# Optimization experiments

Hardware: AMD Instinct MI355X
Metric: run time of the kernel (lower is better)

## Reference

```python
import jax, jax.numpy as jnp
import numpy as np

A0 = 0.5291772105638411
KE = 14.399645351950548


def _softplus_inverse(x):
    return x + np.log(-np.expm1(-x))


def _sigma(x):
    # exp(-1/clamp(x,1e-12)) underflows to 0 for x<=0, so the where is nan-free
    return jnp.where(x > 0, jnp.exp(-1.0 / jnp.maximum(x, 1e-12)), 0.0)


def _switch(x, x_on, x_off):
    c = (x - x_on) / (x_off - x_on)
    s1 = _sigma(1.0 - c)
    s0 = _sigma(c)
    return s1 / (s1 + s0 + 1e-12)


def setup_inputs() -> dict:
    key = jax.random.key(0)
    k0, k1, k2, k3, k4 = jax.random.split(key, 5)
    N = 100000
    E = 6400000
    atomic_numbers = jax.random.uniform(k0, (N,), jnp.float32, 1.0, 30.0)
    cutoffs = jax.random.uniform(k1, (E, 1), jnp.float32)
    lengths = jax.random.uniform(k2, (E, 1), jnp.float32, 0.5, 3.0)
    senders = jax.random.randint(k3, (E,), 0, N)
    receivers = jax.random.randint(k4, (E,), 0, N)
    init = dict(a1=3.2, a2=0.9423, a3=0.4028, a4=0.2016,
                c1=0.1818, c2=0.5099, c3=0.2802, c4=0.02817,
                p=0.23, d=1.0 / (0.8854 * A0))
    params = {k + '_raw': jnp.asarray([_softplus_inverse(v)], jnp.float32)
              for k, v in init.items()}
    out = {'atomic_numbers': atomic_numbers, 'cutoffs': cutoffs,
           'senders': senders, 'receivers': receivers,
           'lengths': lengths, 'num_nodes': N}
    out.update(params)
    return out


def reference(atomic_numbers, cutoffs, senders, receivers, lengths, num_nodes,
              a1_raw, a2_raw, a3_raw, a4_raw,
              c1_raw, c2_raw, c3_raw, c4_raw, p_raw, d_raw):
    sp = jax.nn.softplus
    a1, a2, a3, a4 = sp(a1_raw), sp(a2_raw), sp(a3_raw), sp(a4_raw)
    c1, c2, c3, c4 = sp(c1_raw), sp(c2_raw), sp(c3_raw), sp(c4_raw)
    p, d = sp(p_raw), sp(d_raw)
    c_sum = c1 + c2 + c3 + c4
    c1, c2, c3, c4 = c1 / c_sum, c2 / c_sum, c3 / c_sum, c4 / c_sum

    cut = cutoffs[:, 0]   # [E]
    L = lengths[:, 0]     # [E]
    z_i = atomic_numbers[receivers]
    z_j = atomic_numbers[senders]

    x = KE * cut * (z_i * z_j) / jnp.maximum(L, 1e-6)
    rzd = L * (jnp.power(z_i, p) + jnp.power(z_j, p)) * d
    y = (c1 * jnp.exp(-a1 * rzd) + c2 * jnp.exp(-a2 * rzd)
         + c3 * jnp.exp(-a3 * rzd) + c4 * jnp.exp(-a4 * rzd))
    w = _switch(L, 0.0, 1.5)
    e_rep_edge = w * x * y * 0.5
    return jax.ops.segment_sum(e_rep_edge, receivers, num_segments=num_nodes)[:, None]
```

## Files before the change

### kernel.cpp

```cpp
#include <hip/hip_runtime.h>
#include <math.h>

#define C0KE 7.199822675975274f
#define LOG2E 1.4426950408889634f
#define BSHIFT 8
#define NB 391
#define CAP 8192
#define PAIRS_OFF 2048
#define K1_BLOCKS 512
#define K1_THREADS 1024

__device__ __forceinline__ float softplusf(float x) {
    return (x > 20.0f) ? x : log1pf(__expf(x));
}

struct ZblParams { float A1, A2, A3, A4, c1, c2, c3, c4, p; };

__device__ __forceinline__ void load_params(
    const float* a1r, const float* a2r, const float* a3r, const float* a4r,
    const float* c1r, const float* c2r, const float* c3r, const float* c4r,
    const float* pr, const float* dr, ZblParams* P)
{
    float d  = softplusf(dr[0]);
    float s  = d * LOG2E;
    P->A1 = softplusf(a1r[0]) * s;
    P->A2 = softplusf(a2r[0]) * s;
    P->A3 = softplusf(a3r[0]) * s;
    P->A4 = softplusf(a4r[0]) * s;
    float c1 = softplusf(c1r[0]), c2 = softplusf(c2r[0]);
    float c3 = softplusf(c3r[0]), c4 = softplusf(c4r[0]);
    float inv = 1.0f / (c1 + c2 + c3 + c4);
    P->c1 = c1 * inv; P->c2 = c2 * inv; P->c3 = c3 * inv; P->c4 = c4 * inv;
    P->p = softplusf(pr[0]);
}

__device__ __forceinline__ float edge_energy_fast(
    float l, float cut_, float zi, float zj, const ZblParams& P)
{
    float c  = l * (1.0f / 1.5f);
    float om = 1.0f - c;
    float s1 = __builtin_amdgcn_exp2f(-LOG2E * __builtin_amdgcn_rcpf(om));
    float s0 = __builtin_amdgcn_exp2f(-LOG2E * __builtin_amdgcn_rcpf(c));
    float w  = s1 * __builtin_amdgcn_rcpf(s1 + s0);
    float x  = C0KE * cut_ * zi * zj * __builtin_amdgcn_rcpf(l);
    float S  = __builtin_amdgcn_exp2f(P.p * __builtin_amdgcn_logf(zi))
             + __builtin_amdgcn_exp2f(P.p * __builtin_amdgcn_logf(zj));
    float t  = l * S;
    float y  = P.c1 * __builtin_amdgcn_exp2f(-P.A1 * t)
             + P.c2 * __builtin_amdgcn_exp2f(-P.A2 * t)
             + P.c3 * __builtin_amdgcn_exp2f(-P.A3 * t)
             + P.c4 * __builtin_amdgcn_exp2f(-P.A4 * t);
    return w * x * y;
}

__global__ __launch_bounds__(K1_THREADS, 8) void zbl_scatter(
    const float* __restrict__ z, const float* __restrict__ cut,
    const int* __restrict__ snd, const int* __restrict__ rcv,
    const float* __restrict__ len,
    const float* __restrict__ a1r, const float* __restrict__ a2r,
    const float* __restrict__ a3r, const float* __restrict__ a4r,
    const float* __restrict__ c1r, const float* __restrict__ c2r,
    const float* __restrict__ c3r, const float* __restrict__ c4r,
    const float* __restrict__ pr,  const float* __restrict__ dr,
    float* __restrict__ out, unsigned* __restrict__ cursor,
    unsigned* __restrict__ pairs, int E)
{
    __shared__ ZblParams P;
    __shared__ unsigned hist[NB];
    __shared__ unsigned basearr[NB];

    for (int b = threadIdx.x; b < NB; b += blockDim.x) hist[b] = 0;
    if (threadIdx.x == 0)
        load_params(a1r, a2r, a3r, a4r, c1r, c2r, c3r, c4r, pr, dr, &P);
    __syncthreads();

    int nq = (E + 3) >> 2;
    int qpb = (nq + gridDim.x - 1) / gridDim.x;
    int q0 = blockIdx.x * qpb;
    int q1 = min(q0 + qpb, nq);

    for (int q = q0 + (int)threadIdx.x; q < q1; q += blockDim.x) {
        int base = q * 4;
        if (base + 4 <= E) {
            float4 l4 = ((const float4*)len)[q];
            int4   r4 = ((const int4*)rcv)[q];
            if (l4.x < 1.5f) atomicAdd(&hist[((unsigned)r4.x) >> BSHIFT], 1u);
            if (l4.y < 1.5f) atomicAdd(&hist[((unsigned)r4.y) >> BSHIFT], 1u);
            if (l4.z < 1.5f) atomicAdd(&hist[((unsigned)r4.z) >> BSHIFT], 1u);
            if (l4.w < 1.5f) atomicAdd(&hist[((unsigned)r4.w) >> BSHIFT], 1u);
        } else {
            for (int e = base; e < E; ++e)
                if (len[e] < 1.5f) atomicAdd(&hist[((unsigned)rcv[e]) >> BSHIFT], 1u);
        }
    }
    __syncthreads();

    for (int b = threadIdx.x; b < NB; b += blockDim.x) {
        unsigned c = hist[b];
        basearr[b] = c ? atomicAdd(&cursor[b], c) : 0u;
        hist[b] = 0;
    }
    __syncthreads();

    const ZblParams Pl = P;

    for (int q = q0 + (int)threadIdx.x; q < q1; q += blockDim.x) {
        int base = q * 4;
        float cs[4], Ls[4]; int ss[4], rr[4]; int cnt;
        if (base + 4 <= E) {
            float4 c4v = ((const float4*)cut)[q];
            float4 l4v = ((const float4*)len)[q];
            int4   s4v = ((const int4*)snd)[q];
            int4   r4v = ((const int4*)rcv)[q];
            cs[0]=c4v.x; cs[1]=c4v.y; cs[2]=c4v.z; cs[3]=c4v.w;
            Ls[0]=l4v.x; Ls[1]=l4v.y; Ls[2]=l4v.z; Ls[3]=l4v.w;
            ss[0]=s4v.x; ss[1]=s4v.y; ss[2]=s4v.z; ss[3]=s4v.w;
            rr[0]=r4v.x; rr[1]=r4v.y; rr[2]=r4v.z; rr[3]=r4v.w;
            cnt = 4;
        } else {
            cnt = E - base;
            for (int k = 0; k < cnt; ++k) {
                cs[k] = cut[base+k]; Ls[k] = len[base+k];
                ss[k] = snd[base+k]; rr[k] = rcv[base+k];
            }
        }
        #pragma unroll
        for (int k = 0; k < 4; ++k) {
            if (k >= cnt) break;
            if (Ls[k] < 1.5f) {
                float e_rep = edge_energy_fast(Ls[k], cs[k],
                                               z[rr[k]], z[ss[k]], Pl);
                unsigned b = ((unsigned)rr[k]) >> BSHIFT;
                unsigned slot = basearr[b] + atomicAdd(&hist[b], 1u);
                if (slot < CAP) {
                    unsigned enc = (__float_as_uint(e_rep) & 0xFFFFFF00u)
                                 | ((unsigned)rr[k] & 0xFFu);
                    pairs[(size_t)b * CAP + slot] = enc;
                } else {
                    unsafeAtomicAdd(&out[rr[k]], e_rep);
                }
            }
        }
    }
}

__global__ __launch_bounds__(256) void zbl_gather(
    const unsigned* __restrict__ cursor, const unsigned* __restrict__ pairs,
    float* __restrict__ out, int N)
{
    __shared__ float acc[256];
    acc[threadIdx.x] = 0.0f;
    __syncthreads();

    int b = blockIdx.x;
    unsigned cnt = cursor[b];
    if (cnt > CAP) cnt = CAP;
    const unsigned* p = pairs + (size_t)b * CAP;
    for (unsigned t = threadIdx.x; t < cnt; t += blockDim.x) {
        unsigned e = p[t];
        atomicAdd(&acc[e & 255u], __uint_as_float(e & 0xFFFFFF00u));
    }
    __syncthreads();

    int n = (b << BSHIFT) + threadIdx.x;
    if (n < N)
        out[n] += acc[threadIdx.x];
}

__global__ __launch_bounds__(256) void zbl_direct(
    const float* __restrict__ z, const float* __restrict__ cut,
    const int* __restrict__ snd, const int* __restrict__ rcv,
    const float* __restrict__ len,
    const float* __restrict__ a1r, const float* __restrict__ a2r,
    const float* __restrict__ a3r, const float* __restrict__ a4r,
    const float* __restrict__ c1r, const float* __restrict__ c2r,
    const float* __restrict__ c3r, const float* __restrict__ c4r,
    const float* __restrict__ pr,  const float* __restrict__ dr,
    float* __restrict__ out, int n4, int E)
{
    __shared__ ZblParams P;
    if (threadIdx.x == 0)
        load_params(a1r, a2r, a3r, a4r, c1r, c2r, c3r, c4r, pr, dr, &P);
    __syncthreads();
    const ZblParams Pl = P;

    int i = blockIdx.x * blockDim.x + threadIdx.x;
    if (i >= n4) return;
    int base = i * 4;
    float cs[4], Ls[4]; int ss[4], rr[4]; int cnt;
    if (base + 4 <= E) {
        float4 c4v = ((const float4*)cut)[i];
        float4 l4v = ((const float4*)len)[i];
        int4   s4v = ((const int4*)snd)[i];
        int4   r4v = ((const int4*)rcv)[i];
        cs[0]=c4v.x; cs[1]=c4v.y; cs[2]=c4v.z; cs[3]=c4v.w;
        Ls[0]=l4v.x; Ls[1]=l4v.y; Ls[2]=l4v.z; Ls[3]=l4v.w;
        ss[0]=s4v.x; ss[1]=s4v.y; ss[2]=s4v.z; ss[3]=s4v.w;
        rr[0]=r4v.x; rr[1]=r4v.y; rr[2]=r4v.z; rr[3]=r4v.w;
        cnt = 4;
    } else {
        cnt = E - base;
        for (int k = 0; k < cnt; ++k) {
            cs[k] = cut[base+k]; Ls[k] = len[base+k];
            ss[k] = snd[base+k]; rr[k] = rcv[base+k];
        }
    }
    #pragma unroll
    for (int k = 0; k < 4; ++k) {
        if (k >= cnt) break;
        if (Ls[k] < 1.5f) {
            float e_rep = edge_energy_fast(Ls[k], cs[k], z[rr[k]], z[ss[k]], Pl);
            unsafeAtomicAdd(&out[rr[k]], e_rep);
        }
    }
}

extern "C" void kernel_launch(void* const* d_in, const int* in_sizes, int n_in,
                              void* d_out, int out_size, void* d_ws, size_t ws_size,
                              hipStream_t stream) {
    const float* z   = (const float*)d_in[0];
    const float* cut = (const float*)d_in[1];
    const int*   snd = (const int*)d_in[2];
    const int*   rcv = (const int*)d_in[3];
    const float* len = (const float*)d_in[4];
    const float* a1r = (const float*)d_in[6];
    const float* a2r = (const float*)d_in[7];
    const float* a3r = (const float*)d_in[8];
    const float* a4r = (const float*)d_in[9];
    const float* c1r = (const float*)d_in[10];
    const float* c2r = (const float*)d_in[11];
    const float* c3r = (const float*)d_in[12];
    const float* c4r = (const float*)d_in[13];
    const float* pr  = (const float*)d_in[14];
    const float* dr  = (const float*)d_in[15];

    float* out = (float*)d_out;
    int E = in_sizes[2];
    int N = out_size;

    size_t need = (size_t)PAIRS_OFF + (size_t)NB * CAP * sizeof(unsigned);

    hipMemsetAsync(d_out, 0, (size_t)N * sizeof(float), stream);

    if (ws_size >= need) {
        unsigned* cursor = (unsigned*)d_ws;
        unsigned* pairs = (unsigned*)((char*)d_ws + PAIRS_OFF);
        hipMemsetAsync(d_ws, 0, PAIRS_OFF, stream);

        hipLaunchKernelGGL(zbl_scatter, dim3(K1_BLOCKS), dim3(K1_THREADS), 0, stream,
                           z, cut, snd, rcv, len,
                           a1r, a2r, a3r, a4r, c1r, c2r, c3r, c4r, pr, dr,
                           out, cursor, pairs, E);
        hipLaunchKernelGGL(zbl_gather, dim3(NB), dim3(256), 0, stream,
                           (const unsigned*)cursor, (const unsigned*)pairs, out, N);
    } else {
        int n4 = (E + 3) / 4;
        int blocks = (n4 + 255) / 256;
        hipLaunchKernelGGL(zbl_direct, dim3(blocks), dim3(256), 0, stream,
                           z, cut, snd, rcv, len,
                           a1r, a2r, a3r, a4r, c1r, c2r, c3r, c4r, pr, dr,
                           out, n4, E);
    }
}
```

Before: 240.9 us.

## Bucket edges per block in LDS and reduce via per-block offset tables

Each block now takes a contiguous chunk of edges and builds a local histogram of receiver buckets. A wave-level prefix scan turns it into offsets, and the block sorts its encoded energies into shared memory, then writes them contiguously to a per-block region together with an offset table. The reduce kernel walks all 512 block rows for its bucket and writes the outputs directly. This removes the global cursor atomics, the capacity-overflow fallback with global float atomics, and both memsets. In exchange the reduce does serial per-thread loops over variable-length segments and uses a large LDS buffer (about 50KB), which limits occupancy of the build kernel.

New measurement: 207.3 us. 1.16x faster.

```diff
diff --git a/kernel.cpp b/kernel.cpp
--- a/kernel.cpp
+++ b/kernel.cpp
@@ -5,10 +5,10 @@
 #define LOG2E 1.4426950408889634f
 #define BSHIFT 8
 #define NB 391
-#define CAP 8192
-#define PAIRS_OFF 2048
-#define K1_BLOCKS 512
-#define K1_THREADS 1024
+#define NBP 392
+#define K1B 512
+#define K1T 1024
+#define PLCAP 12512
 
 __device__ __forceinline__ float softplusf(float x) {
     return (x > 20.0f) ? x : log1pf(__expf(x));
@@ -53,7 +53,7 @@
     return w * x * y;
 }
 
-__global__ __launch_bounds__(K1_THREADS, 8) void zbl_scatter(
+__global__ __launch_bounds__(K1T) void zbl_build(
     const float* __restrict__ z, const float* __restrict__ cut,
     const int* __restrict__ snd, const int* __restrict__ rcv,
     const float* __restrict__ len,
@@ -62,109 +62,139 @@
     const float* __restrict__ c1r, const float* __restrict__ c2r,
     const float* __restrict__ c3r, const float* __restrict__ c4r,
     const float* __restrict__ pr,  const float* __restrict__ dr,
-    float* __restrict__ out, unsigned* __restrict__ cursor,
-    unsigned* __restrict__ pairs, int E)
+    unsigned* __restrict__ T,
+    unsigned* __restrict__ Pg,
+    int RSTRIDE, int EPB, int E)
 {
     __shared__ ZblParams P;
-    __shared__ unsigned hist[NB];
-    __shared__ unsigned basearr[NB];
-
-    for (int b = threadIdx.x; b < NB; b += blockDim.x) hist[b] = 0;
-    if (threadIdx.x == 0)
+    __shared__ unsigned chist[NB];
+    __shared__ unsigned cbase[NBP];
+    __shared__ unsigned fillc[NB];
+    __shared__ unsigned wavesum[16];
+    __shared__ unsigned pl[PLCAP];
+
+    const int tid = threadIdx.x;
+    if (tid == 0)
         load_params(a1r, a2r, a3r, a4r, c1r, c2r, c3r, c4r, pr, dr, &P);
-    __syncthreads();
-
-    int nq = (E + 3) >> 2;
-    int qpb = (nq + gridDim.x - 1) / gridDim.x;
-    int q0 = blockIdx.x * qpb;
-    int q1 = min(q0 + qpb, nq);
-
-    for (int q = q0 + (int)threadIdx.x; q < q1; q += blockDim.x) {
-        int base = q * 4;
-        if (base + 4 <= E) {
-            float4 l4 = ((const float4*)len)[q];
-            int4   r4 = ((const int4*)rcv)[q];
-            if (l4.x < 1.5f) atomicAdd(&hist[((unsigned)r4.x) >> BSHIFT], 1u);
-            if (l4.y < 1.5f) atomicAdd(&hist[((unsigned)r4.y) >> BSHIFT], 1u);
-            if (l4.z < 1.5f) atomicAdd(&hist[((unsigned)r4.z) >> BSHIFT], 1u);
-            if (l4.w < 1.5f) atomicAdd(&hist[((unsigned)r4.w) >> BSHIFT], 1u);
-        } else {
-            for (int e = base; e < E; ++e)
-                if (len[e] < 1.5f) atomicAdd(&hist[((unsigned)rcv[e]) >> BSHIFT], 1u);
-        }
-    }
-    __syncthreads();
-
-    for (int b = threadIdx.x; b < NB; b += blockDim.x) {
-        unsigned c = hist[b];
-        basearr[b] = c ? atomicAdd(&cursor[b], c) : 0u;
-        hist[b] = 0;
-    }
-    __syncthreads();
-
+    for (int b = tid; b < NB; b += K1T) { chist[b] = 0u; fillc[b] = 0u; }
+    __syncthreads();
     const ZblParams Pl = P;
 
-    for (int q = q0 + (int)threadIdx.x; q < q1; q += blockDim.x) {
-        int base = q * 4;
-        float cs[4], Ls[4]; int ss[4], rr[4]; int cnt;
-        if (base + 4 <= E) {
-            float4 c4v = ((const float4*)cut)[q];
-            float4 l4v = ((const float4*)len)[q];
-            int4   s4v = ((const int4*)snd)[q];
-            int4   r4v = ((const int4*)rcv)[q];
-            cs[0]=c4v.x; cs[1]=c4v.y; cs[2]=c4v.z; cs[3]=c4v.w;
-            Ls[0]=l4v.x; Ls[1]=l4v.y; Ls[2]=l4v.z; Ls[3]=l4v.w;
-            ss[0]=s4v.x; ss[1]=s4v.y; ss[2]=s4v.z; ss[3]=s4v.w;
-            rr[0]=r4v.x; rr[1]=r4v.y; rr[2]=r4v.z; rr[3]=r4v.w;
-            cnt = 4;
-        } else {
-            cnt = E - base;
-            for (int k = 0; k < cnt; ++k) {
-                cs[k] = cut[base+k]; Ls[k] = len[base+k];
-                ss[k] = snd[base+k]; rr[k] = rcv[base+k];
+    const int blk = blockIdx.x;
+    const int e0 = blk * EPB;
+    const int e1 = min(e0 + EPB, E);
+    const int nv = (e1 > e0) ? ((e1 - e0) >> 2) : 0;
+    const int qb = e0 >> 2;
+    const int etail = e0 + (nv << 2);
+
+    for (int q = tid; q < nv; q += K1T) {
+        float4 l4 = ((const float4*)len)[qb + q];
+        int4   r4 = ((const int4*)rcv)[qb + q];
+        if (l4.x < 1.5f) atomicAdd(&chist[((unsigned)r4.x) >> BSHIFT], 1u);
+        if (l4.y < 1.5f) atomicAdd(&chist[((unsigned)r4.y) >> BSHIFT], 1u);
+        if (l4.z < 1.5f) atomicAdd(&chist[((unsigned)r4.z) >> BSHIFT], 1u);
+        if (l4.w < 1.5f) atomicAdd(&chist[((unsigned)r4.w) >> BSHIFT], 1u);
+    }
+    for (int e = etail + tid; e < e1; e += K1T)
+        if (len[e] < 1.5f) atomicAdd(&chist[((unsigned)rcv[e]) >> BSHIFT], 1u);
+    __syncthreads();
+
+    {
+        const int lane = tid & 63, wv = tid >> 6;
+        unsigned own = (tid < NB) ? chist[tid] : 0u;
+        unsigned v = own;
+        #pragma unroll
+        for (int o = 1; o < 64; o <<= 1) {
+            unsigned u = __shfl_up(v, o);
+            if (lane >= o) v += u;
+        }
+        if (lane == 63 && wv < 7) wavesum[wv] = v;
+        __syncthreads();
+        if (wv == 0) {
+            unsigned s = (lane < 7) ? wavesum[lane] : 0u;
+            #pragma unroll
+            for (int o = 1; o < 8; o <<= 1) {
+                unsigned u = __shfl_up(s, o);
+                if (lane >= o) s += u;
             }
-        }
-        #pragma unroll
-        for (int k = 0; k < 4; ++k) {
-            if (k >= cnt) break;
-            if (Ls[k] < 1.5f) {
-                float e_rep = edge_energy_fast(Ls[k], cs[k],
-                                               z[rr[k]], z[ss[k]], Pl);
-                unsigned b = ((unsigned)rr[k]) >> BSHIFT;
-                unsigned slot = basearr[b] + atomicAdd(&hist[b], 1u);
-                if (slot < CAP) {
-                    unsigned enc = (__float_as_uint(e_rep) & 0xFFFFFF00u)
-                                 | ((unsigned)rr[k] & 0xFFu);
-                    pairs[(size_t)b * CAP + slot] = enc;
-                } else {
-                    unsafeAtomicAdd(&out[rr[k]], e_rep);
+            if (lane < 7) wavesum[lane] = s;
+        }
+        __syncthreads();
+        unsigned off = (wv > 0 && wv < 8) ? wavesum[wv - 1] : 0u;
+        if (tid < NB) cbase[tid] = off + v - own;
+        if (tid == 0) cbase[NB] = wavesum[6];
+    }
+    __syncthreads();
+
+    const unsigned blkbase = (unsigned)blk * (unsigned)RSTRIDE;
+    const unsigned trow = (unsigned)blk * (unsigned)NBP;
+    for (int b = tid; b <= NB; b += K1T)
+        T[trow + b] = blkbase + cbase[b];
+
+    for (int q = tid; q < nv; q += K1T) {
+        float4 l4 = ((const float4*)len)[qb + q];
+        if (l4.x < 1.5f || l4.y < 1.5f || l4.z < 1.5f || l4.w < 1.5f) {
+            float4 c4 = ((const float4*)cut)[qb + q];
+            int4   s4 = ((const int4*)snd)[qb + q];
+            int4   r4 = ((const int4*)rcv)[qb + q];
+            float Ls[4] = {l4.x, l4.y, l4.z, l4.w};
+            float Cs[4] = {c4.x, c4.y, c4.z, c4.w};
+            int   Ss[4] = {s4.x, s4.y, s4.z, s4.w};
+            int   Rs[4] = {r4.x, r4.y, r4.z, r4.w};
+            #pragma unroll
+            for (int k = 0; k < 4; ++k) {
+                if (Ls[k] < 1.5f) {
+                    unsigned r = (unsigned)Rs[k];
+                    float v = edge_energy_fast(Ls[k], Cs[k],
+                                               z[r], z[(unsigned)Ss[k]], Pl);
+                    unsigned bk = r >> BSHIFT;
+                    unsigned tk = atomicAdd(&fillc[bk], 1u);
+                    pl[cbase[bk] + tk] = (__float_as_uint(v) & 0xFFFFFF00u)
+                                       | (r & 0xFFu);
                 }
             }
         }
     }
-}
-
-__global__ __launch_bounds__(256) void zbl_gather(
-    const unsigned* __restrict__ cursor, const unsigned* __restrict__ pairs,
+    for (int e = etail + tid; e < e1; e += K1T) {
+        float l = len[e];
+        if (l < 1.5f) {
+            unsigned r = (unsigned)rcv[e];
+            float v = edge_energy_fast(l, cut[e], z[r], z[(unsigned)snd[e]], Pl);
+            unsigned bk = r >> BSHIFT;
+            unsigned tk = atomicAdd(&fillc[bk], 1u);
+            pl[cbase[bk] + tk] = (__float_as_uint(v) & 0xFFFFFF00u) | (r & 0xFFu);
+        }
+    }
+    __syncthreads();
+
+    const unsigned csum = cbase[NB];
+    for (unsigned s = tid; s < csum; s += K1T)
+        Pg[blkbase + s] = pl[s];
+}
+
+__global__ __launch_bounds__(512) void zbl_reduce(
+    const unsigned* __restrict__ T, const unsigned* __restrict__ Pg,
     float* __restrict__ out, int N)
 {
     __shared__ float acc[256];
-    acc[threadIdx.x] = 0.0f;
-    __syncthreads();
-
-    int b = blockIdx.x;
-    unsigned cnt = cursor[b];
-    if (cnt > CAP) cnt = CAP;
-    const unsigned* p = pairs + (size_t)b * CAP;
-    for (unsigned t = threadIdx.x; t < cnt; t += blockDim.x) {
-        unsigned e = p[t];
-        atomicAdd(&acc[e & 255u], __uint_as_float(e & 0xFFFFFF00u));
-    }
-    __syncthreads();
-
-    int n = (b << BSHIFT) + threadIdx.x;
-    if (n < N)
-        out[n] += acc[threadIdx.x];
+    const int tid = threadIdx.x;
+    if (tid < 256) acc[tid] = 0.0f;
+    __syncthreads();
+
+    const int b = blockIdx.x;
+    for (int r = tid; r < K1B; r += 512) {
+        const unsigned* row = T + (size_t)r * NBP;
+        unsigned s = row[b];
+        unsigned e = row[b + 1];
+        for (unsigned i = s; i < e; ++i) {
+            unsigned p = Pg[i];
+            atomicAdd(&acc[p & 255u], __uint_as_float(p & 0xFFFFFF00u));
+        }
+    }
+    __syncthreads();
+
+    int n = (b << BSHIFT) + tid;
+    if (tid < 256 && n < N) out[n] = acc[tid];
 }
 
 __global__ __launch_bounds__(256) void zbl_direct(
@@ -238,22 +268,22 @@
     int E = in_sizes[2];
     int N = out_size;
 
-    size_t need = (size_t)PAIRS_OFF + (size_t)NB * CAP * sizeof(unsigned);
-
-    hipMemsetAsync(d_out, 0, (size_t)N * sizeof(float), stream);
-
-    if (ws_size >= need) {
-        unsigned* cursor = (unsigned*)d_ws;
-        unsigned* pairs = (unsigned*)((char*)d_ws + PAIRS_OFF);
-        hipMemsetAsync(d_ws, 0, PAIRS_OFF, stream);
-
-        hipLaunchKernelGGL(zbl_scatter, dim3(K1_BLOCKS), dim3(K1_THREADS), 0, stream,
+    int EPB = (((E + K1B - 1) / K1B) + 3) & ~3;
+    int RSTRIDE = (EPB + 15) & ~15;
+    size_t tsz = ((size_t)K1B * NBP * sizeof(unsigned) + 255) & ~(size_t)255;
+    size_t need1 = tsz + (size_t)K1B * RSTRIDE * sizeof(unsigned);
+
+    if (EPB <= PLCAP && ws_size >= need1) {
+        unsigned* T  = (unsigned*)d_ws;
+        unsigned* Pg = (unsigned*)((char*)d_ws + tsz);
+        hipLaunchKernelGGL(zbl_build, dim3(K1B), dim3(K1T), 0, stream,
                            z, cut, snd, rcv, len,
                            a1r, a2r, a3r, a4r, c1r, c2r, c3r, c4r, pr, dr,
-                           out, cursor, pairs, E);
-        hipLaunchKernelGGL(zbl_gather, dim3(NB), dim3(256), 0, stream,
-                           (const unsigned*)cursor, (const unsigned*)pairs, out, N);
+                           T, Pg, RSTRIDE, EPB, E);
+        hipLaunchKernelGGL(zbl_reduce, dim3(NB), dim3(512), 0, stream,
+                           (const unsigned*)T, (const unsigned*)Pg, out, N);
     } else {
+        hipMemsetAsync(d_out, 0, (size_t)N * sizeof(float), stream);
         int n4 = (E + 3) / 4;
         int blocks = (n4 + 255) / 256;
         hipLaunchKernelGGL(zbl_direct, dim3(blocks), dim3(256), 0, stream,
```
